# Performance work log

Measured on AMD Instinct MI355X. Metric: run time of the kernel, lower is better.

Reference implementation:

```python
import jax, jax.numpy as jnp
import numpy as np

WS = 25          # window_size
THRESHOLD = 3.5  # default threshold in find_low_quality_regions


def _conv1d_gelu(x, w, b, pad):
    # x: (N, C_in, L), w: (C_out, C_in, K) -> gelu(conv(x) + b), SAME length
    y = jax.lax.conv_general_dilated(
        x, w, window_strides=(1,), padding=[(pad, pad)],
        dimension_numbers=("NCH", "OIH", "NCH"))
    return jax.nn.gelu(y + b[None, :, None], approximate=False)


def setup_inputs() -> dict:
    key = jax.random.key(0)
    ks = jax.random.split(key, 12)
    B, T, D, H = 8, 25000, 256, 128
    s = 0.05
    return {
        "latents": jax.random.normal(ks[0], (B, T, D), jnp.float32),
        "conv0_w": jax.random.normal(ks[1], (H, D, 7), jnp.float32) * s,
        "conv0_b": jax.random.normal(ks[2], (H,), jnp.float32) * s,
        "conv1_w": jax.random.normal(ks[3], (H, H, 5), jnp.float32) * s,
        "conv1_b": jax.random.normal(ks[4], (H,), jnp.float32) * s,
        "conv2_w": jax.random.normal(ks[5], (H, H, 5), jnp.float32) * s,
        "conv2_b": jax.random.normal(ks[6], (H,), jnp.float32) * s,
        "head_w1": jax.random.normal(ks[7], (H, H), jnp.float32) * s,
        "head_b1": jax.random.normal(ks[8], (H,), jnp.float32) * s,
        "head_w2": jax.random.normal(ks[9], (1, H), jnp.float32) * s,
        "head_b2": jax.random.normal(ks[10], (1,), jnp.float32) * s,
    }


def reference(latents, conv0_w, conv0_b, conv1_w, conv1_b, conv2_w, conv2_b,
              head_w1, head_b1, head_w2, head_b2):
    B, T, D = latents.shape
    nw = (T - WS) // WS + 1  # number of non-overlapping windows
    # (B, nw, WS, D) -> (B*nw, D, WS): batch all windows through the critic
    x = latents[:, :nw * WS].reshape(B, nw, WS, D).reshape(B * nw, WS, D)
    x = jnp.transpose(x, (0, 2, 1))  # NCH
    x = _conv1d_gelu(x, conv0_w, conv0_b, pad=3)
    x = _conv1d_gelu(x, conv1_w, conv1_b, pad=2)
    x = _conv1d_gelu(x, conv2_w, conv2_b, pad=2)
    feat = x.mean(axis=2)  # AdaptiveAvgPool1d(1) -> (B*nw, H)
    h = jax.nn.gelu(feat @ head_w1.T + head_b1, approximate=False)
    score = jax.nn.sigmoid(h @ head_w2.T + head_b2)[:, 0] * 5.0  # (B*nw,)
    scores = score.reshape(B, nw).mean(axis=0)  # critic(window).mean() per window
    low_quality = scores < THRESHOLD  # windows the loop would append as regions
    return scores, low_quality
```

## Files before the change

### kernel.cpp

```cpp
#include <hip/hip_runtime.h>
#include <math.h>

#define BATCH 8
#define T_LEN 25000
#define NW    1000
#define WS    25
#define D0    256
#define H     128

typedef __bf16 bf16;
typedef bf16 bf16x8 __attribute__((ext_vector_type(8)));
typedef bf16 bf16x4 __attribute__((ext_vector_type(4)));
typedef float f32x4 __attribute__((ext_vector_type(4)));

__device__ __forceinline__ float gelu_fast(float x) {
    float y = 0.7978845608f * x * (1.0f + 0.044715f * x * x);
    float e = __expf(2.0f * y);
    float t = 1.0f - 2.0f * __builtin_amdgcn_rcpf(e + 1.0f);
    return 0.5f * x * (1.0f + t);
}

__device__ __forceinline__ void repack_one(const float* __restrict__ w,
                                           bf16* __restrict__ dst, int idx,
                                           int Cin, int K, int KSn) {
    int j    = idx & 7;
    int lane = (idx >> 3) & 63;
    int mt   = (idx >> 9) & 7;
    int ks   = (idx >> 12) % KSn;
    int k    = idx / (4096 * KSn);
    int co = mt * 16 + (lane & 15);
    int ci = ks * 32 + (lane >> 4) * 8 + j;
    dst[idx] = (bf16)w[(co * Cin + ci) * K + k];
}

__global__ void prep_kernel(const float* __restrict__ c0w, const float* __restrict__ c1w,
                            const float* __restrict__ c2w, const float* __restrict__ hw1,
                            bf16* __restrict__ p0, bf16* __restrict__ p1,
                            bf16* __restrict__ p2, bf16* __restrict__ hw1b) {
    int t = blockIdx.x * 256 + threadIdx.x;
    if (t < 229376) {
        repack_one(c0w, p0, t, 256, 7, 8);
    } else if (t < 311296) {
        repack_one(c1w, p1, t - 229376, 128, 5, 4);
    } else if (t < 393216) {
        repack_one(c2w, p2, t - 311296, 128, 5, 4);
    } else if (t < 409600) {
        int i = t - 393216;
        hw1b[i] = (bf16)hw1[i];
    }
}

#define XT_LD 264
#define A_LD  136
#define OFF_A2   33456
#define OFF_FEAT 70752
#define OFF_H    72800
#define SMEM_BYTES 74848

__global__ __launch_bounds__(256, 2)
void critic_kernel(const float* __restrict__ lat,
                   const bf16* __restrict__ p0, const float* __restrict__ b0,
                   const bf16* __restrict__ p1, const float* __restrict__ b1,
                   const bf16* __restrict__ p2, const float* __restrict__ b2,
                   const bf16* __restrict__ hw1b, const float* __restrict__ hb1,
                   const float* __restrict__ hw2, const float* __restrict__ hb2,
                   float* __restrict__ scores_tmp) {
    __shared__ __align__(16) char smem[SMEM_BYTES];
    bf16  (*xT)[XT_LD]  = (bf16(*)[XT_LD])smem;
    bf16  (*a1T)[A_LD]  = (bf16(*)[A_LD])smem;
    bf16  (*a2T)[A_LD]  = (bf16(*)[A_LD])(smem + OFF_A2);
    float* feat = (float*)(smem + OFF_FEAT);
    float* hbuf = (float*)(smem + OFF_H);

    const int tid = threadIdx.x;
    const int bx  = blockIdx.x;
    const int b   = bx / (NW / 4);
    const int wi  = bx % (NW / 4);
    const int w0  = 4 * wi;

    {
        const float4* src4 = (const float4*)(lat + ((size_t)b * T_LEN + (size_t)w0 * WS) * D0);
        #pragma unroll
        for (int it = 0; it < 25; ++it) {
            int g = tid + it * 256;
            int l = g >> 6, c0 = (g & 63) * 4;
            int win = l / 25, lr = l - win * 25;
            int r = 31 * win + lr + 3;
            float4 v = src4[g];
            bf16x4 o = {(bf16)v.x, (bf16)v.y, (bf16)v.z, (bf16)v.w};
            *(bf16x4*)&xT[r][c0] = o;
        }
        bf16x4 z4 = {};
        #pragma unroll
        for (int it = 0; it < 6; ++it) {
            int i = tid + it * 256;
            int rr = i >> 6, c0 = (i & 63) * 4;
            int j = rr / 6, t6 = rr - 6 * j;
            int r = 31 * j + ((t6 < 3) ? t6 : t6 + 25);
            *(bf16x4*)&xT[r][c0] = z4;
        }
    }
    __syncthreads();

    const int lane = tid & 63, wv = tid >> 6;
    const int m = lane & 15, q = lane >> 4;
    const bf16* xb  = &xT[m][q * 8];
    const bf16* a1b = &a1T[m][q * 8];

    f32x4 acc[2][8] = {};
    {
        const bf16x8* A = (const bf16x8*)p0 + (size_t)wv * 64 + lane;
        #pragma unroll
        for (int k = 0; k < 7; ++k) {
            #pragma unroll
            for (int ks = 0; ks < 8; ++ks) {
                bf16x8 a0 = A[(k * 8 + ks) * 512];
                bf16x8 a1 = A[(k * 8 + ks) * 512 + 256];
                #pragma unroll
                for (int win = 0; win < 4; ++win) {
                    const bf16* pB = xb + (k + 31 * win) * XT_LD + ks * 32;
                    bf16x8 bb0 = *(const bf16x8*)(pB);
                    bf16x8 bb1 = *(const bf16x8*)(pB + 16 * XT_LD);
                    acc[0][2 * win]     = __builtin_amdgcn_mfma_f32_16x16x32_bf16(a0, bb0, acc[0][2 * win], 0, 0, 0);
                    acc[0][2 * win + 1] = __builtin_amdgcn_mfma_f32_16x16x32_bf16(a0, bb1, acc[0][2 * win + 1], 0, 0, 0);
                    acc[1][2 * win]     = __builtin_amdgcn_mfma_f32_16x16x32_bf16(a1, bb0, acc[1][2 * win], 0, 0, 0);
                    acc[1][2 * win + 1] = __builtin_amdgcn_mfma_f32_16x16x32_bf16(a1, bb1, acc[1][2 * win + 1], 0, 0, 0);
                }
            }
        }
    }
    __syncthreads();
    {
        bf16x4 z4 = {};
        #pragma unroll
        for (int it = 0; it < 4; ++it) {
            int i = tid + it * 256;
            int arr = i >> 9, rr = (i >> 5) & 15, c0 = (i & 31) * 4;
            int j = rr >> 2, t4 = rr & 3;
            int r = 29 * j + ((t4 < 2) ? t4 : t4 + 25);
            if (arr == 0) *(bf16x4*)&a1T[r][c0] = z4;
            else          *(bf16x4*)&a2T[r][c0] = z4;
        }
    }
    #pragma unroll
    for (int mt = 0; mt < 2; ++mt) {
        int co0 = (wv + 4 * mt) * 16 + q * 4;
        f32x4 bv = *(const f32x4*)&b0[co0];
        #pragma unroll
        for (int win = 0; win < 4; ++win) {
            #pragma unroll
            for (int nt = 0; nt < 2; ++nt) {
                int l = nt * 16 + m;
                if (l < 25) {
                    bf16x4 v;
                    #pragma unroll
                    for (int r = 0; r < 4; ++r)
                        v[r] = (bf16)gelu_fast(acc[mt][2 * win + nt][r] + bv[r]);
                    *(bf16x4*)&a1T[l + 2 + 29 * win][co0] = v;
                }
            }
        }
    }
    __syncthreads();

    f32x4 c1[2][8] = {};
    {
        const bf16x8* A = (const bf16x8*)p1 + (size_t)wv * 64 + lane;
        #pragma unroll
        for (int k = 0; k < 5; ++k) {
            #pragma unroll
            for (int ks = 0; ks < 4; ++ks) {
                bf16x8 a0 = A[(k * 4 + ks) * 512];
                bf16x8 a1 = A[(k * 4 + ks) * 512 + 256];
                #pragma unroll
                for (int win = 0; win < 4; ++win) {
                    const bf16* pB = a1b + (k + 29 * win) * A_LD + ks * 32;
                    bf16x8 bb0 = *(const bf16x8*)(pB);
                    bf16x8 bb1 = *(const bf16x8*)(pB + 16 * A_LD);
                    c1[0][2 * win]     = __builtin_amdgcn_mfma_f32_16x16x32_bf16(a0, bb0, c1[0][2 * win], 0, 0, 0);
                    c1[0][2 * win + 1] = __builtin_amdgcn_mfma_f32_16x16x32_bf16(a0, bb1, c1[0][2 * win + 1], 0, 0, 0);
                    c1[1][2 * win]     = __builtin_amdgcn_mfma_f32_16x16x32_bf16(a1, bb0, c1[1][2 * win], 0, 0, 0);
                    c1[1][2 * win + 1] = __builtin_amdgcn_mfma_f32_16x16x32_bf16(a1, bb1, c1[1][2 * win + 1], 0, 0, 0);
                }
            }
        }
    }
    #pragma unroll
    for (int mt = 0; mt < 2; ++mt) {
        int co0 = (wv + 4 * mt) * 16 + q * 4;
        f32x4 bv = *(const f32x4*)&b1[co0];
        #pragma unroll
        for (int win = 0; win < 4; ++win) {
            #pragma unroll
            for (int nt = 0; nt < 2; ++nt) {
                int l = nt * 16 + m;
                if (l < 25) {
                    bf16x4 v;
                    #pragma unroll
                    for (int r = 0; r < 4; ++r)
                        v[r] = (bf16)gelu_fast(c1[mt][2 * win + nt][r] + bv[r]);
                    *(bf16x4*)&a2T[l + 2 + 29 * win][co0] = v;
                }
            }
        }
    }
    __syncthreads();

    f32x4 c2[2][8] = {};
    {
        const bf16* a2b = &a2T[m][q * 8];
        const bf16x8* A = (const bf16x8*)p2 + (size_t)wv * 64 + lane;
        #pragma unroll
        for (int k = 0; k < 5; ++k) {
            #pragma unroll
            for (int ks = 0; ks < 4; ++ks) {
                bf16x8 a0 = A[(k * 4 + ks) * 512];
                bf16x8 a1 = A[(k * 4 + ks) * 512 + 256];
                #pragma unroll
                for (int win = 0; win < 4; ++win) {
                    const bf16* pB = a2b + (k + 29 * win) * A_LD + ks * 32;
                    bf16x8 bb0 = *(const bf16x8*)(pB);
                    bf16x8 bb1 = *(const bf16x8*)(pB + 16 * A_LD);
                    c2[0][2 * win]     = __builtin_amdgcn_mfma_f32_16x16x32_bf16(a0, bb0, c2[0][2 * win], 0, 0, 0);
                    c2[0][2 * win + 1] = __builtin_amdgcn_mfma_f32_16x16x32_bf16(a0, bb1, c2[0][2 * win + 1], 0, 0, 0);
                    c2[1][2 * win]     = __builtin_amdgcn_mfma_f32_16x16x32_bf16(a1, bb0, c2[1][2 * win], 0, 0, 0);
                    c2[1][2 * win + 1] = __builtin_amdgcn_mfma_f32_16x16x32_bf16(a1, bb1, c2[1][2 * win + 1], 0, 0, 0);
                }
            }
        }
    }
    #pragma unroll
    for (int mt = 0; mt < 2; ++mt) {
        int co0 = (wv + 4 * mt) * 16 + q * 4;
        f32x4 bv = *(const f32x4*)&b2[co0];
        #pragma unroll
        for (int win = 0; win < 4; ++win) {
            f32x4 pool;
            #pragma unroll
            for (int r = 0; r < 4; ++r) {
                float s  = gelu_fast(c2[mt][2 * win][r] + bv[r]);
                float g1 = gelu_fast(c2[mt][2 * win + 1][r] + bv[r]);
                s += (m < 9) ? g1 : 0.0f;
                s += __shfl_xor(s, 1);
                s += __shfl_xor(s, 2);
                s += __shfl_xor(s, 4);
                s += __shfl_xor(s, 8);
                pool[r] = s * 0.04f;
            }
            if (m == 0) *(f32x4*)&feat[win * 128 + co0] = pool;
        }
    }
    __syncthreads();

    {
        int wb = tid >> 7, co = tid & 127;
        const bf16x8* row = (const bf16x8*)(hw1b + co * H);
        const float* f0 = feat + wb * 128;
        const float* f1 = feat + (wb + 2) * 128;
        float a0h = hb1[co], a1h = a0h;
        #pragma unroll
        for (int jv = 0; jv < 16; ++jv) {
            bf16x8 w8 = row[jv];
            #pragma unroll
            for (int u = 0; u < 8; ++u) {
                float wf = (float)w8[u];
                a0h += wf * f0[jv * 8 + u];
                a1h += wf * f1[jv * 8 + u];
            }
        }
        hbuf[wb * 128 + co] = gelu_fast(a0h);
        hbuf[(wb + 2) * 128 + co] = gelu_fast(a1h);
    }
    __syncthreads();

    {
        int win = tid >> 6, j = tid & 63;
        const float* hb = hbuf + win * 128;
        float p = hw2[j] * hb[j] + hw2[j + 64] * hb[j + 64];
        #pragma unroll
        for (int off = 32; off > 0; off >>= 1) p += __shfl_down(p, off);
        if (j == 0) {
            float z = p + hb2[0];
            scores_tmp[b * NW + w0 + win] = 5.0f / (1.0f + expf(-z));
        }
    }
}

__global__ void finalize_kernel(const float* __restrict__ tmp, float* __restrict__ out) {
    int w = blockIdx.x * 256 + threadIdx.x;
    if (w < NW) {
        float s = 0.0f;
        #pragma unroll
        for (int b = 0; b < BATCH; ++b) s += tmp[b * NW + w];
        s *= 0.125f;
        out[w] = s;
        out[NW + w] = (s < 3.5f) ? 1.0f : 0.0f;
    }
}

extern "C" void kernel_launch(void* const* d_in, const int* in_sizes, int n_in,
                              void* d_out, int out_size, void* d_ws, size_t ws_size,
                              hipStream_t stream) {
    const float* lat  = (const float*)d_in[0];
    const float* c0w  = (const float*)d_in[1];
    const float* c0b  = (const float*)d_in[2];
    const float* c1w  = (const float*)d_in[3];
    const float* c1b  = (const float*)d_in[4];
    const float* c2w  = (const float*)d_in[5];
    const float* c2b  = (const float*)d_in[6];
    const float* hw1  = (const float*)d_in[7];
    const float* hb1  = (const float*)d_in[8];
    const float* hw2  = (const float*)d_in[9];
    const float* hb2  = (const float*)d_in[10];

    bf16* p0   = (bf16*)d_ws;
    bf16* p1   = (bf16*)((char*)d_ws + 458752);
    bf16* p2   = (bf16*)((char*)d_ws + 622592);
    bf16* hw1b = (bf16*)((char*)d_ws + 786432);
    float* tmp = (float*)((char*)d_ws + 819200);

    prep_kernel<<<1600, 256, 0, stream>>>(c0w, c1w, c2w, hw1, p0, p1, p2, hw1b);
    critic_kernel<<<BATCH * (NW / 4), 256, 0, stream>>>(lat, p0, c0b, p1, c1b, p2, c2b,
                                                        hw1b, hb1, hw2, hb2, tmp);
    finalize_kernel<<<4, 256, 0, stream>>>(tmp, (float*)d_out);
}
```

Measured before the change: 464.3 us.

## Split critic work across eight waves, one window per wave

Doubles the block to 512 threads so each wave computes one window across 64 output channels, instead of all four windows across 32 channels. Per-wave accumulator state drops from sixteen to eight MFMA tiles, and the aim is more latency hiding per block. In exchange, each wave reuses a loaded weight fragment for only two MFMAs rather than eight, which raises weight-fetch traffic. The launch bound of four 512-thread blocks also constrains registers hard, even though the shared-memory footprint (about 73 KB per block) likely caps residency at two blocks anyway, so register spills are a risk.

```diff
diff --git a/kernel.cpp b/kernel.cpp
--- a/kernel.cpp
+++ b/kernel.cpp
@@ -57,7 +57,7 @@
 #define OFF_H    72800
 #define SMEM_BYTES 74848
 
-__global__ __launch_bounds__(256, 2)
+__global__ __launch_bounds__(512, 4)
 void critic_kernel(const float* __restrict__ lat,
                    const bf16* __restrict__ p0, const float* __restrict__ b0,
                    const bf16* __restrict__ p1, const float* __restrict__ b1,
@@ -81,19 +81,21 @@
     {
         const float4* src4 = (const float4*)(lat + ((size_t)b * T_LEN + (size_t)w0 * WS) * D0);
         #pragma unroll
-        for (int it = 0; it < 25; ++it) {
-            int g = tid + it * 256;
-            int l = g >> 6, c0 = (g & 63) * 4;
-            int win = l / 25, lr = l - win * 25;
-            int r = 31 * win + lr + 3;
-            float4 v = src4[g];
-            bf16x4 o = {(bf16)v.x, (bf16)v.y, (bf16)v.z, (bf16)v.w};
-            *(bf16x4*)&xT[r][c0] = o;
+        for (int it = 0; it < 13; ++it) {
+            int g = tid + it * 512;
+            if (g < 6400) {
+                int l = g >> 6, c0 = (g & 63) * 4;
+                int win = l / 25, lr = l - win * 25;
+                int r = 31 * win + lr + 3;
+                float4 v = src4[g];
+                bf16x4 o = {(bf16)v.x, (bf16)v.y, (bf16)v.z, (bf16)v.w};
+                *(bf16x4*)&xT[r][c0] = o;
+            }
         }
         bf16x4 z4 = {};
         #pragma unroll
-        for (int it = 0; it < 6; ++it) {
-            int i = tid + it * 256;
+        for (int it = 0; it < 3; ++it) {
+            int i = tid + it * 512;
             int rr = i >> 6, c0 = (i & 63) * 4;
             int j = rr / 6, t6 = rr - 6 * j;
             int r = 31 * j + ((t6 < 3) ? t6 : t6 + 25);
@@ -103,29 +105,31 @@
     __syncthreads();
 
     const int lane = tid & 63, wv = tid >> 6;
+    const int win = wv & 3, mtg = wv >> 2;
     const int m = lane & 15, q = lane >> 4;
     const bf16* xb  = &xT[m][q * 8];
     const bf16* a1b = &a1T[m][q * 8];
 
-    f32x4 acc[2][8] = {};
-    {
-        const bf16x8* A = (const bf16x8*)p0 + (size_t)wv * 64 + lane;
+    f32x4 acc[4][2] = {};
+    {
+        const bf16x8* A = (const bf16x8*)p0 + (size_t)mtg * 256 + lane;
         #pragma unroll
         for (int k = 0; k < 7; ++k) {
             #pragma unroll
             for (int ks = 0; ks < 8; ++ks) {
-                bf16x8 a0 = A[(k * 8 + ks) * 512];
-                bf16x8 a1 = A[(k * 8 + ks) * 512 + 256];
-                #pragma unroll
-                for (int win = 0; win < 4; ++win) {
-                    const bf16* pB = xb + (k + 31 * win) * XT_LD + ks * 32;
-                    bf16x8 bb0 = *(const bf16x8*)(pB);
-                    bf16x8 bb1 = *(const bf16x8*)(pB + 16 * XT_LD);
-                    acc[0][2 * win]     = __builtin_amdgcn_mfma_f32_16x16x32_bf16(a0, bb0, acc[0][2 * win], 0, 0, 0);
-                    acc[0][2 * win + 1] = __builtin_amdgcn_mfma_f32_16x16x32_bf16(a0, bb1, acc[0][2 * win + 1], 0, 0, 0);
-                    acc[1][2 * win]     = __builtin_amdgcn_mfma_f32_16x16x32_bf16(a1, bb0, acc[1][2 * win], 0, 0, 0);
-                    acc[1][2 * win + 1] = __builtin_amdgcn_mfma_f32_16x16x32_bf16(a1, bb1, acc[1][2 * win + 1], 0, 0, 0);
-                }
+                int f = (k * 8 + ks) * 512;
+                bf16x8 a0 = A[f], a1 = A[f + 64], a2 = A[f + 128], a3 = A[f + 192];
+                const bf16* pB = xb + (k + 31 * win) * XT_LD + ks * 32;
+                bf16x8 bb0 = *(const bf16x8*)(pB);
+                bf16x8 bb1 = *(const bf16x8*)(pB + 16 * XT_LD);
+                acc[0][0] = __builtin_amdgcn_mfma_f32_16x16x32_bf16(a0, bb0, acc[0][0], 0, 0, 0);
+                acc[0][1] = __builtin_amdgcn_mfma_f32_16x16x32_bf16(a0, bb1, acc[0][1], 0, 0, 0);
+                acc[1][0] = __builtin_amdgcn_mfma_f32_16x16x32_bf16(a1, bb0, acc[1][0], 0, 0, 0);
+                acc[1][1] = __builtin_amdgcn_mfma_f32_16x16x32_bf16(a1, bb1, acc[1][1], 0, 0, 0);
+                acc[2][0] = __builtin_amdgcn_mfma_f32_16x16x32_bf16(a2, bb0, acc[2][0], 0, 0, 0);
+                acc[2][1] = __builtin_amdgcn_mfma_f32_16x16x32_bf16(a2, bb1, acc[2][1], 0, 0, 0);
+                acc[3][0] = __builtin_amdgcn_mfma_f32_16x16x32_bf16(a3, bb0, acc[3][0], 0, 0, 0);
+                acc[3][1] = __builtin_amdgcn_mfma_f32_16x16x32_bf16(a3, bb1, acc[3][1], 0, 0, 0);
             }
         }
     }
@@ -133,8 +137,8 @@
     {
         bf16x4 z4 = {};
         #pragma unroll
-        for (int it = 0; it < 4; ++it) {
-            int i = tid + it * 256;
+        for (int it = 0; it < 2; ++it) {
+            int i = tid + it * 512;
             int arr = i >> 9, rr = (i >> 5) & 15, c0 = (i & 31) * 4;
             int j = rr >> 2, t4 = rr & 3;
             int r = 29 * j + ((t4 < 2) ? t4 : t4 + 25);
@@ -143,112 +147,105 @@
         }
     }
     #pragma unroll
-    for (int mt = 0; mt < 2; ++mt) {
-        int co0 = (wv + 4 * mt) * 16 + q * 4;
+    for (int i = 0; i < 4; ++i) {
+        int co0 = (mtg * 4 + i) * 16 + q * 4;
         f32x4 bv = *(const f32x4*)&b0[co0];
         #pragma unroll
-        for (int win = 0; win < 4; ++win) {
-            #pragma unroll
-            for (int nt = 0; nt < 2; ++nt) {
-                int l = nt * 16 + m;
-                if (l < 25) {
-                    bf16x4 v;
-                    #pragma unroll
-                    for (int r = 0; r < 4; ++r)
-                        v[r] = (bf16)gelu_fast(acc[mt][2 * win + nt][r] + bv[r]);
-                    *(bf16x4*)&a1T[l + 2 + 29 * win][co0] = v;
-                }
-            }
-        }
-    }
-    __syncthreads();
-
-    f32x4 c1[2][8] = {};
-    {
-        const bf16x8* A = (const bf16x8*)p1 + (size_t)wv * 64 + lane;
+        for (int nt = 0; nt < 2; ++nt) {
+            int l = nt * 16 + m;
+            if (l < 25) {
+                bf16x4 v;
+                #pragma unroll
+                for (int r = 0; r < 4; ++r)
+                    v[r] = (bf16)gelu_fast(acc[i][nt][r] + bv[r]);
+                *(bf16x4*)&a1T[l + 2 + 29 * win][co0] = v;
+            }
+        }
+    }
+    __syncthreads();
+
+    f32x4 c1[4][2] = {};
+    {
+        const bf16x8* A = (const bf16x8*)p1 + (size_t)mtg * 256 + lane;
         #pragma unroll
         for (int k = 0; k < 5; ++k) {
             #pragma unroll
             for (int ks = 0; ks < 4; ++ks) {
-                bf16x8 a0 = A[(k * 4 + ks) * 512];
-                bf16x8 a1 = A[(k * 4 + ks) * 512 + 256];
+                int f = (k * 4 + ks) * 512;
+                bf16x8 a0 = A[f], a1 = A[f + 64], a2 = A[f + 128], a3 = A[f + 192];
+                const bf16* pB = a1b + (k + 29 * win) * A_LD + ks * 32;
+                bf16x8 bb0 = *(const bf16x8*)(pB);
+                bf16x8 bb1 = *(const bf16x8*)(pB + 16 * A_LD);
+                c1[0][0] = __builtin_amdgcn_mfma_f32_16x16x32_bf16(a0, bb0, c1[0][0], 0, 0, 0);
+                c1[0][1] = __builtin_amdgcn_mfma_f32_16x16x32_bf16(a0, bb1, c1[0][1], 0, 0, 0);
+                c1[1][0] = __builtin_amdgcn_mfma_f32_16x16x32_bf16(a1, bb0, c1[1][0], 0, 0, 0);
+                c1[1][1] = __builtin_amdgcn_mfma_f32_16x16x32_bf16(a1, bb1, c1[1][1], 0, 0, 0);
+                c1[2][0] = __builtin_amdgcn_mfma_f32_16x16x32_bf16(a2, bb0, c1[2][0], 0, 0, 0);
+                c1[2][1] = __builtin_amdgcn_mfma_f32_16x16x32_bf16(a2, bb1, c1[2][1], 0, 0, 0);
+                c1[3][0] = __builtin_amdgcn_mfma_f32_16x16x32_bf16(a3, bb0, c1[3][0], 0, 0, 0);
+                c1[3][1] = __builtin_amdgcn_mfma_f32_16x16x32_bf16(a3, bb1, c1[3][1], 0, 0, 0);
+            }
+        }
+    }
+    #pragma unroll
+    for (int i = 0; i < 4; ++i) {
+        int co0 = (mtg * 4 + i) * 16 + q * 4;
+        f32x4 bv = *(const f32x4*)&b1[co0];
+        #pragma unroll
+        for (int nt = 0; nt < 2; ++nt) {
+            int l = nt * 16 + m;
+            if (l < 25) {
+                bf16x4 v;
                 #pragma unroll
-                for (int win = 0; win < 4; ++win) {
-                    const bf16* pB = a1b + (k + 29 * win) * A_LD + ks * 32;
-                    bf16x8 bb0 = *(const bf16x8*)(pB);
-                    bf16x8 bb1 = *(const bf16x8*)(pB + 16 * A_LD);
-                    c1[0][2 * win]     = __builtin_amdgcn_mfma_f32_16x16x32_bf16(a0, bb0, c1[0][2 * win], 0, 0, 0);
-                    c1[0][2 * win + 1] = __builtin_amdgcn_mfma_f32_16x16x32_bf16(a0, bb1, c1[0][2 * win + 1], 0, 0, 0);
-                    c1[1][2 * win]     = __builtin_amdgcn_mfma_f32_16x16x32_bf16(a1, bb0, c1[1][2 * win], 0, 0, 0);
-                    c1[1][2 * win + 1] = __builtin_amdgcn_mfma_f32_16x16x32_bf16(a1, bb1, c1[1][2 * win + 1], 0, 0, 0);
-                }
-            }
-        }
-    }
-    #pragma unroll
-    for (int mt = 0; mt < 2; ++mt) {
-        int co0 = (wv + 4 * mt) * 16 + q * 4;
-        f32x4 bv = *(const f32x4*)&b1[co0];
-        #pragma unroll
-        for (int win = 0; win < 4; ++win) {
-            #pragma unroll
-            for (int nt = 0; nt < 2; ++nt) {
-                int l = nt * 16 + m;
-                if (l < 25) {
-                    bf16x4 v;
-                    #pragma unroll
-                    for (int r = 0; r < 4; ++r)
-                        v[r] = (bf16)gelu_fast(c1[mt][2 * win + nt][r] + bv[r]);
-                    *(bf16x4*)&a2T[l + 2 + 29 * win][co0] = v;
-                }
-            }
-        }
-    }
-    __syncthreads();
-
-    f32x4 c2[2][8] = {};
+                for (int r = 0; r < 4; ++r)
+                    v[r] = (bf16)gelu_fast(c1[i][nt][r] + bv[r]);
+                *(bf16x4*)&a2T[l + 2 + 29 * win][co0] = v;
+            }
+        }
+    }
+    __syncthreads();
+
+    f32x4 c2[4][2] = {};
     {
         const bf16* a2b = &a2T[m][q * 8];
-        const bf16x8* A = (const bf16x8*)p2 + (size_t)wv * 64 + lane;
+        const bf16x8* A = (const bf16x8*)p2 + (size_t)mtg * 256 + lane;
         #pragma unroll
         for (int k = 0; k < 5; ++k) {
             #pragma unroll
             for (int ks = 0; ks < 4; ++ks) {
-                bf16x8 a0 = A[(k * 4 + ks) * 512];
-                bf16x8 a1 = A[(k * 4 + ks) * 512 + 256];
-                #pragma unroll
-                for (int win = 0; win < 4; ++win) {
-                    const bf16* pB = a2b + (k + 29 * win) * A_LD + ks * 32;
-                    bf16x8 bb0 = *(const bf16x8*)(pB);
-                    bf16x8 bb1 = *(const bf16x8*)(pB + 16 * A_LD);
-                    c2[0][2 * win]     = __builtin_amdgcn_mfma_f32_16x16x32_bf16(a0, bb0, c2[0][2 * win], 0, 0, 0);
-                    c2[0][2 * win + 1] = __builtin_amdgcn_mfma_f32_16x16x32_bf16(a0, bb1, c2[0][2 * win + 1], 0, 0, 0);
-                    c2[1][2 * win]     = __builtin_amdgcn_mfma_f32_16x16x32_bf16(a1, bb0, c2[1][2 * win], 0, 0, 0);
-                    c2[1][2 * win + 1] = __builtin_amdgcn_mfma_f32_16x16x32_bf16(a1, bb1, c2[1][2 * win + 1], 0, 0, 0);
-                }
+                int f = (k * 4 + ks) * 512;
+                bf16x8 a0 = A[f], a1 = A[f + 64], a2 = A[f + 128], a3 = A[f + 192];
+                const bf16* pB = a2b + (k + 29 * win) * A_LD + ks * 32;
+                bf16x8 bb0 = *(const bf16x8*)(pB);
+                bf16x8 bb1 = *(const bf16x8*)(pB + 16 * A_LD);
+                c2[0][0] = __builtin_amdgcn_mfma_f32_16x16x32_bf16(a0, bb0, c2[0][0], 0, 0, 0);
+                c2[0][1] = __builtin_amdgcn_mfma_f32_16x16x32_bf16(a0, bb1, c2[0][1], 0, 0, 0);
+                c2[1][0] = __builtin_amdgcn_mfma_f32_16x16x32_bf16(a1, bb0, c2[1][0], 0, 0, 0);
+                c2[1][1] = __builtin_amdgcn_mfma_f32_16x16x32_bf16(a1, bb1, c2[1][1], 0, 0, 0);
+                c2[2][0] = __builtin_amdgcn_mfma_f32_16x16x32_bf16(a2, bb0, c2[2][0], 0, 0, 0);
+                c2[2][1] = __builtin_amdgcn_mfma_f32_16x16x32_bf16(a2, bb1, c2[2][1], 0, 0, 0);
+                c2[3][0] = __builtin_amdgcn_mfma_f32_16x16x32_bf16(a3, bb0, c2[3][0], 0, 0, 0);
+                c2[3][1] = __builtin_amdgcn_mfma_f32_16x16x32_bf16(a3, bb1, c2[3][1], 0, 0, 0);
             }
         }
     }
     #pragma unroll
-    for (int mt = 0; mt < 2; ++mt) {
-        int co0 = (wv + 4 * mt) * 16 + q * 4;
+    for (int i = 0; i < 4; ++i) {
+        int co0 = (mtg * 4 + i) * 16 + q * 4;
         f32x4 bv = *(const f32x4*)&b2[co0];
-        #pragma unroll
-        for (int win = 0; win < 4; ++win) {
-            f32x4 pool;
-            #pragma unroll
-            for (int r = 0; r < 4; ++r) {
-                float s  = gelu_fast(c2[mt][2 * win][r] + bv[r]);
-                float g1 = gelu_fast(c2[mt][2 * win + 1][r] + bv[r]);
-                s += (m < 9) ? g1 : 0.0f;
-                s += __shfl_xor(s, 1);
-                s += __shfl_xor(s, 2);
-                s += __shfl_xor(s, 4);
-                s += __shfl_xor(s, 8);
-                pool[r] = s * 0.04f;
-            }
-            if (m == 0) *(f32x4*)&feat[win * 128 + co0] = pool;
-        }
+        f32x4 pool;
+        #pragma unroll
+        for (int r = 0; r < 4; ++r) {
+            float s  = gelu_fast(c2[i][0][r] + bv[r]);
+            float g1 = gelu_fast(c2[i][1][r] + bv[r]);
+            s += (m < 9) ? g1 : 0.0f;
+            s += __shfl_xor(s, 1);
+            s += __shfl_xor(s, 2);
+            s += __shfl_xor(s, 4);
+            s += __shfl_xor(s, 8);
+            pool[r] = s * 0.04f;
+        }
+        if (m == 0) *(f32x4*)&feat[win * 128 + co0] = pool;
     }
     __syncthreads();
 
@@ -256,32 +253,27 @@
         int wb = tid >> 7, co = tid & 127;
         const bf16x8* row = (const bf16x8*)(hw1b + co * H);
         const float* f0 = feat + wb * 128;
-        const float* f1 = feat + (wb + 2) * 128;
-        float a0h = hb1[co], a1h = a0h;
+        float a0h = hb1[co];
         #pragma unroll
         for (int jv = 0; jv < 16; ++jv) {
             bf16x8 w8 = row[jv];
             #pragma unroll
-            for (int u = 0; u < 8; ++u) {
-                float wf = (float)w8[u];
-                a0h += wf * f0[jv * 8 + u];
-                a1h += wf * f1[jv * 8 + u];
-            }
+            for (int u = 0; u < 8; ++u)
+                a0h += (float)w8[u] * f0[jv * 8 + u];
         }
         hbuf[wb * 128 + co] = gelu_fast(a0h);
-        hbuf[(wb + 2) * 128 + co] = gelu_fast(a1h);
-    }
-    __syncthreads();
-
-    {
-        int win = tid >> 6, j = tid & 63;
-        const float* hb = hbuf + win * 128;
+    }
+    __syncthreads();
+
+    if (tid < 256) {
+        int win2 = tid >> 6, j = tid & 63;
+        const float* hb = hbuf + win2 * 128;
         float p = hw2[j] * hb[j] + hw2[j + 64] * hb[j + 64];
         #pragma unroll
         for (int off = 32; off > 0; off >>= 1) p += __shfl_down(p, off);
         if (j == 0) {
             float z = p + hb2[0];
-            scores_tmp[b * NW + w0 + win] = 5.0f / (1.0f + expf(-z));
+            scores_tmp[b * NW + w0 + win2] = 5.0f / (1.0f + expf(-z));
         }
     }
 }
@@ -320,7 +312,7 @@
     float* tmp = (float*)((char*)d_ws + 819200);
 
     prep_kernel<<<1600, 256, 0, stream>>>(c0w, c1w, c2w, hw1, p0, p1, p2, hw1b);
-    critic_kernel<<<BATCH * (NW / 4), 256, 0, stream>>>(lat, p0, c0b, p1, c1b, p2, c2b,
+    critic_kernel<<<BATCH * (NW / 4), 512, 0, stream>>>(lat, p0, c0b, p1, c1b, p2, c2b,
                                                         hw1b, hb1, hw2, hb2, tmp);
     finalize_kernel<<<4, 256, 0, stream>>>(tmp, (float*)d_out);
 }
```

After: 526.6 us. 1.13x slower.
